# Performance work log

Hardware: AMD Instinct MI355X
Metric: run time of the kernel (lower is better)

The kernel has to match this reference:

```python
import jax, jax.numpy as jnp
import numpy as np

N, IN_F, OUT_F, H = 8192, 256, 64, 4
NEG_SLOPE = 0.2


def setup_inputs() -> dict:
    key = jax.random.key(0)
    ks = jax.random.split(key, 8)
    inputs = jax.random.normal(ks[0], (N, IN_F), dtype=jnp.float32)
    # sparse-ish binary adjacency with self loops (sparse.softmax only sees nonzeros)
    adj = (jax.random.uniform(ks[1], (N, N)) < 0.05).astype(jnp.float32)
    idx = jnp.arange(N)
    adj = adj.at[idx, idx].set(1.0)
    stdv = 1.0 / np.sqrt(H * OUT_F)
    weight = jax.random.uniform(ks[2], (IN_F, H * OUT_F), minval=-stdv, maxval=stdv, dtype=jnp.float32)
    bias = jax.random.uniform(ks[3], (1, H * OUT_F), minval=-stdv, maxval=stdv, dtype=jnp.float32)
    # weight_u/v: stdv = 1/sqrt(size(-1)=1) = 1
    weight_u = jax.random.uniform(ks[4], (H, OUT_F, 1), minval=-1.0, maxval=1.0, dtype=jnp.float32)
    weight_v = jax.random.uniform(ks[5], (H, OUT_F, 1), minval=-1.0, maxval=1.0, dtype=jnp.float32)
    stdp = 1.0 / np.sqrt(IN_F)
    proj_w = jax.random.uniform(ks[6], (H * OUT_F, IN_F), minval=-stdp, maxval=stdp, dtype=jnp.float32)
    proj_b = jax.random.uniform(ks[7], (H * OUT_F,), minval=-stdp, maxval=stdp, dtype=jnp.float32)
    return {"inputs": inputs, "adj_mat": adj, "weight": weight, "weight_u": weight_u,
            "weight_v": weight_v, "bias": bias, "proj_w": proj_w, "proj_b": proj_b}


def reference(inputs, adj_mat, weight, weight_u, weight_v, bias, proj_w, proj_b):
    n = inputs.shape[0]
    support = (inputs @ weight).reshape(n, H, OUT_F).transpose(1, 0, 2)  # [H,N,O]
    f1 = jnp.einsum('hno,ho->hn', support, weight_u[..., 0])  # [H,N]
    f2 = jnp.einsum('hno,ho->hn', support, weight_v[..., 0])  # [H,N]
    logits = f1[:, None, :] + f2[:, :, None]                  # [H,N,N]
    w = jax.nn.leaky_relu(logits, NEG_SLOPE)
    masked = w * adj_mat                                      # adj broadcast over heads
    mask = adj_mat != 0.0
    # sparse.softmax over dim 2: softmax restricted to nonzero (edge) positions
    neg = jnp.where(mask, masked, -jnp.inf)
    m = jnp.max(neg, axis=2, keepdims=True)
    m = jnp.where(jnp.isfinite(m), m, 0.0)
    e = jnp.where(mask, jnp.exp(neg - m), 0.0)
    denom = jnp.sum(e, axis=2, keepdims=True)
    attn = e / jnp.where(denom > 0, denom, 1.0)               # [H,N,N]
    out = jnp.einsum('hnm,hmo->hno', attn, support)           # [H,N,O]
    out = out.transpose(1, 0, 2).reshape(n, H * OUT_F)
    out = out + bias
    out = out + inputs @ proj_w.T + proj_b
    return out
```

## Files before the change

### kernel.cpp

```cpp
#include <hip/hip_runtime.h>
#include <hip/hip_bf16.h>

#define N_NODES 8192
#define IN_FEAT 256
#define OUT_F   64
#define NHEAD   4
#define HF      256
#define NEG     0.2f

typedef unsigned short u16;
typedef unsigned char  u8;
typedef unsigned long long u64;
typedef _Float16 h2    __attribute__((ext_vector_type(2)));
typedef _Float16 half8 __attribute__((ext_vector_type(8)));
typedef __attribute__((ext_vector_type(4))) float f32x4;

__global__ __launch_bounds__(256) void k_tr(const float* __restrict__ PW,
                                            float* __restrict__ PWT) {
    __shared__ float t[64][65];
    const int bx = (blockIdx.x & 3) * 64;
    const int by = (blockIdx.x >> 2) * 64;
    const int tx = threadIdx.x & 63;
    const int ty = threadIdx.x >> 6;
    #pragma unroll
    for (int r = ty; r < 64; r += 4)
        t[r][tx] = PW[(size_t)(by + r) * IN_FEAT + bx + tx];
    __syncthreads();
    #pragma unroll
    for (int r = ty; r < 64; r += 4)
        PWT[(size_t)(bx + r) * HF + by + tx] = t[tx][r];
}

#define RPB 4
__global__ __launch_bounds__(256, 8) void k_gemm(
    const float* __restrict__ inp,
    const float* __restrict__ W,
    const float* __restrict__ U,
    const float* __restrict__ V,
    const float* __restrict__ Bias,
    const float* __restrict__ PWT,
    const float* __restrict__ PB,
    const float* __restrict__ adj,
    _Float16* __restrict__ suppB,
    float* __restrict__ f1,
    float* __restrict__ f2,
    float* __restrict__ outp,
    unsigned* __restrict__ gb32,
    float* __restrict__ anum,
    float* __restrict__ aden)
{
    __shared__ __align__(16) float in_lds[RPB][IN_FEAT];
    const int c  = threadIdx.x;
    const int n0 = blockIdx.x * RPB;

    #pragma unroll
    for (int r = 0; r < RPB; ++r)
        in_lds[r][c] = inp[(size_t)(n0 + r) * IN_FEAT + c];
    __syncthreads();

    float accs[RPB], accp[RPB];
    #pragma unroll
    for (int r = 0; r < RPB; ++r) { accs[r] = 0.f; accp[r] = 0.f; }

    const float* wc = W   + c;
    const float* pc = PWT + c;
    float w0 = wc[0 * HF], w1 = wc[1 * HF], w2 = wc[2 * HF], w3 = wc[3 * HF];
    float p0 = pc[0 * HF], p1 = pc[1 * HF], p2 = pc[2 * HF], p3 = pc[3 * HF];

    #pragma unroll 1
    for (int k = 0; k < IN_FEAT; k += 4) {
        const int kn = (k + 4) & 255;
        const float nw0 = wc[(kn + 0) * HF];
        const float nw1 = wc[(kn + 1) * HF];
        const float nw2 = wc[(kn + 2) * HF];
        const float nw3 = wc[(kn + 3) * HF];
        const float np0 = pc[(kn + 0) * HF];
        const float np1 = pc[(kn + 1) * HF];
        const float np2 = pc[(kn + 2) * HF];
        const float np3 = pc[(kn + 3) * HF];
        #pragma unroll
        for (int r = 0; r < RPB; ++r) {
            const float4 xv = *(const float4*)&in_lds[r][k];
            accs[r] = fmaf(xv.x, w0, accs[r]);
            accs[r] = fmaf(xv.y, w1, accs[r]);
            accs[r] = fmaf(xv.z, w2, accs[r]);
            accs[r] = fmaf(xv.w, w3, accs[r]);
            accp[r] = fmaf(xv.x, p0, accp[r]);
            accp[r] = fmaf(xv.y, p1, accp[r]);
            accp[r] = fmaf(xv.z, p2, accp[r]);
            accp[r] = fmaf(xv.w, p3, accp[r]);
        }
        w0 = nw0; w1 = nw1; w2 = nw2; w3 = nw3;
        p0 = np0; p1 = np1; p2 = np2; p3 = np3;
    }

    const int h = c >> 6, lane = c & 63;
    const float uv = U[c], vv = V[c];
    const float bb = Bias[c] + PB[c];

    {
        const int o   = c & 63;
        const int t   = o >> 4;
        const int cc  = o & 15;
        const int jbg = n0 >> 5;
        const int q   = (n0 & 31) >> 3;
        const int el  = n0 & 7;
        union { _Float16 hh[4]; u64 q8; } sv;
        #pragma unroll
        for (int r = 0; r < RPB; ++r) sv.hh[r] = (_Float16)accs[r];
        const size_t word = ((size_t)(h * 256 + jbg) * 4 + t) * 64 + (q << 4) + cc;
        *(u64*)(suppB + word * 8 + el) = sv.q8;
    }

    #pragma unroll
    for (int r = 0; r < RPB; ++r) {
        float s1 = accs[r] * uv, s2 = accs[r] * vv;
        #pragma unroll
        for (int mm = 32; mm > 0; mm >>= 1) {
            s1 += __shfl_xor(s1, mm);
            s2 += __shfl_xor(s2, mm);
        }
        if (lane == 0) {
            f1[h * N_NODES + n0 + r] = s1;
            f2[h * N_NODES + n0 + r] = s2;
        }
        outp[(size_t)(n0 + r) * HF + c] = accp[r] + bb;
    }

    #pragma unroll
    for (int r = 0; r < RPB; ++r)
        anum[(size_t)(n0 + r) * HF + c] = 0.f;
    if (c < 16)
        aden[(size_t)(c >> 2) * N_NODES + n0 + (c & 3)] = 0.f;

    #pragma unroll
    for (int r = 0; r < RPB; ++r) {
        const float* ar = adj + (size_t)(n0 + r) * N_NODES;
        unsigned wrd = 0;
        #pragma unroll
        for (int p = 0; p < 4; ++p) {
            const int j = c * 32 + p * 8;
            const float4 a0 = *(const float4*)(ar + j);
            const float4 a1 = *(const float4*)(ar + j + 4);
            const unsigned b =
                (unsigned)(a0.x != 0.f)        | ((unsigned)(a0.y != 0.f) << 1) |
                ((unsigned)(a0.z != 0.f) << 2) | ((unsigned)(a0.w != 0.f) << 3) |
                ((unsigned)(a1.x != 0.f) << 4) | ((unsigned)(a1.y != 0.f) << 5) |
                ((unsigned)(a1.z != 0.f) << 6) | ((unsigned)(a1.w != 0.f) << 7);
            wrd |= b << (8 * p);
        }
        gb32[(size_t)(n0 + r) * 256 + c] = wrd;
    }
}

__global__ __launch_bounds__(256) void k_prep(const float* __restrict__ f1,
                                              float* __restrict__ f1max,
                                              _Float16* __restrict__ EA16,
                                              _Float16* __restrict__ EB16) {
    __shared__ float red[256];
    const int h = blockIdx.x;
    float m = -1e30f;
    for (int j = threadIdx.x; j < N_NODES; j += 256)
        m = fmaxf(m, f1[h * N_NODES + j]);
    red[threadIdx.x] = m;
    __syncthreads();
    for (int s = 128; s > 0; s >>= 1) {
        if (threadIdx.x < s) red[threadIdx.x] = fmaxf(red[threadIdx.x], red[threadIdx.x + s]);
        __syncthreads();
    }
    const float fm = red[0];
    if (threadIdx.x == 0) f1max[h] = fm;
    for (int j = threadIdx.x; j < N_NODES; j += 256) {
        const float d = f1[h * N_NODES + j] - fm;
        EA16[(size_t)h * N_NODES + j] = (_Float16)__expf(d);
        EB16[(size_t)h * N_NODES + j] = (_Float16)__expf(NEG * d);
    }
}

#define TI 64
#define NSUB 4
#define JSPLIT_G 4
#define JW (N_NODES / JSPLIT_G)

__global__ __launch_bounds__(256, 3) void k_attn_mfma(
    const unsigned* __restrict__ gb32,
    const _Float16* __restrict__ suppB,
    const _Float16* __restrict__ EA16,
    const _Float16* __restrict__ EB16,
    const float* __restrict__ f2,
    const float* __restrict__ f1max,
    float* __restrict__ anum,
    float* __restrict__ aden)
{
    __shared__ __align__(16) _Float16 ea_lds[NHEAD][JW];
    __shared__ __align__(16) _Float16 eb_lds[NHEAD][JW];
    __shared__ __align__(4)  u8 abyte[TI][260];

    const int itile = blockIdx.x >> 2;
    const int jwin  = blockIdx.x & 3;
    const int i0    = itile * TI;
    const int J0    = jwin * JW;
    const int wv    = threadIdx.x >> 6;
    const int lane  = threadIdx.x & 63;
    const int col   = lane & 15;
    const int quad  = lane >> 4;

    {
        const _Float16* gea = EA16 + (size_t)wv * N_NODES + J0;
        const _Float16* geb = EB16 + (size_t)wv * N_NODES + J0;
        #pragma unroll
        for (int it = 0; it < 4; ++it) {
            const int off = it * 512 + lane * 8;
            *(float4*)&ea_lds[wv][off] = *(const float4*)(gea + off);
            *(float4*)&eb_lds[wv][off] = *(const float4*)(geb + off);
        }
    }
    #pragma unroll
    for (int rr = 0; rr < 16; ++rr) {
        const int r = (wv << 4) + rr;
        *(unsigned*)&abyte[r][lane * 4] =
            gb32[(size_t)(i0 + r) * 256 + (J0 >> 5) + lane];
    }
    __syncthreads();

    const int h = wv;
    const float fm = f1max[h];
    h2 caH[NSUB], cbH[NSUB];
    float ls[NSUB];
    #pragma unroll
    for (int s = 0; s < NSUB; ++s) {
        const float f2i = f2[(size_t)h * N_NODES + i0 + s * 16 + col];
        const float g  = fm + f2i;
        const float mi = fmaxf(g, NEG * g);
        const _Float16 ca = (_Float16)__expf(g - mi);
        const _Float16 cb = (_Float16)__expf(NEG * g - mi);
        caH[s][0] = ca; caH[s][1] = ca;
        cbH[s][0] = cb; cbH[s][1] = cb;
        ls[s] = 0.f;
    }
    const h2 ones = {(_Float16)1.0f, (_Float16)1.0f};

    const _Float16* sb = suppB + (size_t)h * 524288
                       + (size_t)(J0 >> 5) * 2048 + lane * 8;

    f32x4 acc[NSUB][4];
    #pragma unroll
    for (int s = 0; s < NSUB; ++s)
        #pragma unroll
        for (int t = 0; t < 4; ++t)
            acc[s][t] = (f32x4){0.f, 0.f, 0.f, 0.f};

    const int qo = quad << 3;

    #pragma unroll 2
    for (int jb = 0; jb < JW; jb += 32) {
        const int jl = jb + qo;
        const _Float16* fp = sb + (size_t)(jb >> 5) * 2048;
        const half8 bv0 = *(const half8*)(fp);
        const half8 bv1 = *(const half8*)(fp + 512);
        const half8 bv2 = *(const half8*)(fp + 1024);
        const half8 bv3 = *(const half8*)(fp + 1536);

        union { half8 v; h2 pr[4]; } ea, eb;
        ea.v = *(const half8*)&ea_lds[h][jl];
        eb.v = *(const half8*)&eb_lds[h][jl];
        const int wo = (jb >> 3) + quad;

        #pragma unroll
        for (int s = 0; s < NSUB; ++s) {
            const unsigned gw = abyte[col + s * 16][wo];
            union { half8 v; unsigned w[4]; h2 pr[4]; } af;
            #pragma unroll
            for (int p = 0; p < 4; ++p) {
                const h2 pa = ea.pr[p] * caH[s];
                const h2 pb = eb.pr[p] * cbH[s];
                const h2 x  = __builtin_elementwise_max(pa, pb);
                const unsigned mlo = (unsigned)((int)(gw << (31 - 2 * p)) >> 31) & 0x0000FFFFu;
                const unsigned mhi = (unsigned)((int)(gw << (30 - 2 * p)) >> 31) & 0xFFFF0000u;
                union { h2 hh; unsigned u; } xu;
                xu.hh = x;
                xu.u &= (mlo | mhi);
                af.w[p] = xu.u;
                ls[s] = __builtin_amdgcn_fdot2(xu.hh, ones, ls[s], false);
            }
            acc[s][0] = __builtin_amdgcn_mfma_f32_16x16x32_f16(af.v, bv0, acc[s][0], 0, 0, 0);
            acc[s][1] = __builtin_amdgcn_mfma_f32_16x16x32_f16(af.v, bv1, acc[s][1], 0, 0, 0);
            acc[s][2] = __builtin_amdgcn_mfma_f32_16x16x32_f16(af.v, bv2, acc[s][2], 0, 0, 0);
            acc[s][3] = __builtin_amdgcn_mfma_f32_16x16x32_f16(af.v, bv3, acc[s][3], 0, 0, 0);
        }
    }

    #pragma unroll
    for (int s = 0; s < NSUB; ++s) {
        ls[s] += __shfl_xor(ls[s], 16);
        ls[s] += __shfl_xor(ls[s], 32);
    }
    if (quad == 0) {
        #pragma unroll
        for (int s = 0; s < NSUB; ++s)
            unsafeAtomicAdd(aden + (size_t)h * N_NODES + i0 + s * 16 + col, ls[s]);
    }

    #pragma unroll
    for (int s = 0; s < NSUB; ++s) {
        #pragma unroll
        for (int reg = 0; reg < 4; ++reg) {
            const int irow = (quad << 2) + reg;
            float* ap = anum + (size_t)(i0 + s * 16 + irow) * HF + (h << 6) + col;
            #pragma unroll
            for (int t = 0; t < 4; ++t)
                unsafeAtomicAdd(ap + (t << 4), acc[s][t][reg]);
        }
    }
}

__global__ __launch_bounds__(256) void k_fin(const float* __restrict__ anum,
                                             const float* __restrict__ aden,
                                             float* __restrict__ out) {
    const int c = threadIdx.x;
    const int h = c >> 6;
    #pragma unroll
    for (int rr = 0; rr < 4; ++rr) {
        const int n = blockIdx.x * 4 + rr;
        out[(size_t)n * HF + c] += anum[(size_t)n * HF + c]
                                 / aden[(size_t)h * N_NODES + n];
    }
}

extern "C" void kernel_launch(void* const* d_in, const int* in_sizes, int n_in,
                              void* d_out, int out_size, void* d_ws, size_t ws_size,
                              hipStream_t stream) {
    const float* inp  = (const float*)d_in[0];
    const float* adj  = (const float*)d_in[1];
    const float* W    = (const float*)d_in[2];
    const float* U    = (const float*)d_in[3];
    const float* V    = (const float*)d_in[4];
    const float* Bias = (const float*)d_in[5];
    const float* PW   = (const float*)d_in[6];
    const float* PB   = (const float*)d_in[7];
    float* out = (float*)d_out;

    char* ws = (char*)d_ws;
    _Float16* suppB = (_Float16*)(ws);
    float* f1    = (float*)(ws + (4u << 20));
    float* f2    = (float*)(ws + (4u << 20) + (128u << 10));
    float* f1mx  = (float*)(ws + (4u << 20) + (256u << 10));
    float* PWT   = (float*)(ws + (4u << 20) + (320u << 10));
    _Float16* EA16 = (_Float16*)(ws + (4u << 20) + (576u << 10));
    _Float16* EB16 = (_Float16*)(ws + (4u << 20) + (704u << 10));
    float* aden  = (float*)(ws + (4u << 20) + (832u << 10));
    unsigned* gb32 = (unsigned*)(ws + (8u << 20));
    float* anum  = (float*)(ws + (24u << 20));

    k_tr<<<16, 256, 0, stream>>>(PW, PWT);
    k_gemm<<<N_NODES / RPB, 256, 0, stream>>>(inp, W, U, V, Bias, PWT, PB, adj,
                                              suppB, f1, f2, out, gb32, anum, aden);
    k_prep<<<NHEAD, 256, 0, stream>>>(f1, f1mx, EA16, EB16);
    k_attn_mfma<<<(N_NODES / TI) * JSPLIT_G, 256, 0, stream>>>(
        gb32, suppB, EA16, EB16, f2, f1mx, anum, aden);
    k_fin<<<N_NODES / 4, 256, 0, stream>>>(anum, aden, out);
}
```

Baseline: 517.3 us.

## Move projection GEMMs to fp16 MFMA and split adjacency bitpacking into ballot kernel

Replaces the scalar fp32 FMA GEMM (support and projection) with fp16 MFMA 16x16x32, adding kernels that convert inputs to fp16 and pack W and proj_w into an MFMA-friendly layout. Adjacency bitmask construction moves into its own kernel using wavefront ballots, and zeroing of accumulators moves into the input conversion kernel. The aim is to cut the compute cost of the dense GEMM and to simplify the bitmask pass. In exchange it adds launches and lowers the GEMM to fp16 precision, including the residual projection path.

```diff
diff --git a/kernel.cpp b/kernel.cpp
--- a/kernel.cpp
+++ b/kernel.cpp
@@ -10,146 +10,174 @@
 
 typedef unsigned short u16;
 typedef unsigned char  u8;
+typedef unsigned int   u32;
 typedef unsigned long long u64;
 typedef _Float16 h2    __attribute__((ext_vector_type(2)));
 typedef _Float16 half8 __attribute__((ext_vector_type(8)));
 typedef __attribute__((ext_vector_type(4))) float f32x4;
 
-__global__ __launch_bounds__(256) void k_tr(const float* __restrict__ PW,
-                                            float* __restrict__ PWT) {
-    __shared__ float t[64][65];
-    const int bx = (blockIdx.x & 3) * 64;
-    const int by = (blockIdx.x >> 2) * 64;
-    const int tx = threadIdx.x & 63;
-    const int ty = threadIdx.x >> 6;
-    #pragma unroll
-    for (int r = ty; r < 64; r += 4)
-        t[r][tx] = PW[(size_t)(by + r) * IN_FEAT + bx + tx];
-    __syncthreads();
-    #pragma unroll
-    for (int r = ty; r < 64; r += 4)
-        PWT[(size_t)(bx + r) * HF + by + tx] = t[tx][r];
-}
-
-#define RPB 4
-__global__ __launch_bounds__(256, 8) void k_gemm(
-    const float* __restrict__ inp,
-    const float* __restrict__ W,
+__global__ __launch_bounds__(256) void k_x16(const float* __restrict__ inp,
+                                             _Float16* __restrict__ X16,
+                                             float* __restrict__ anum,
+                                             float* __restrict__ aden) {
+    const int i = blockIdx.x * 256 + threadIdx.x;
+    const float4 v = ((const float4*)inp)[i];
+    union { _Float16 hh[4]; u64 q; } cv;
+    cv.hh[0] = (_Float16)v.x; cv.hh[1] = (_Float16)v.y;
+    cv.hh[2] = (_Float16)v.z; cv.hh[3] = (_Float16)v.w;
+    ((u64*)X16)[i] = cv.q;
+    ((float4*)anum)[i] = (float4){0.f, 0.f, 0.f, 0.f};
+    if (i < 8192) ((float4*)aden)[i] = (float4){0.f, 0.f, 0.f, 0.f};
+}
+
+__global__ __launch_bounds__(256) void k_wpack(const float* __restrict__ W,
+                                               const float* __restrict__ PW,
+                                               _Float16* __restrict__ W16B) {
+    const int w = blockIdx.x * 256 + threadIdx.x;
+    const int ks = w >> 11;
+    const int T  = (w >> 6) & 31;
+    const int lane = w & 63;
+    const int q  = lane >> 4, cc = lane & 15;
+    const int n  = T * 16 + cc;
+    const int k0 = ks * 32 + q * 8;
+    union { _Float16 hh[8]; half8 v; } o;
+    #pragma unroll
+    for (int e = 0; e < 8; ++e) {
+        const int k = k0 + e;
+        const float s = (n < 256) ? W[k * 256 + n] : PW[(size_t)(n - 256) * 256 + k];
+        o.hh[e] = (_Float16)s;
+    }
+    *(half8*)(W16B + (size_t)w * 8) = o.v;
+}
+
+__global__ __launch_bounds__(256) void k_bits(const float* __restrict__ adj,
+                                              u64* __restrict__ gb64) {
+    const int row  = blockIdx.x * 4 + (threadIdx.x >> 6);
+    const int lane = threadIdx.x & 63;
+    const float* ar = adj + (size_t)row * N_NODES;
+    u64* gr = gb64 + (size_t)row * 128;
+    #pragma unroll 1
+    for (int it = 0; it < 32; ++it) {
+        const int jb = it * 256;
+        const float a0 = ar[jb + lane];
+        const float a1 = ar[jb + 64 + lane];
+        const float a2 = ar[jb + 128 + lane];
+        const float a3 = ar[jb + 192 + lane];
+        const u64 b0 = __ballot(a0 != 0.f);
+        const u64 b1 = __ballot(a1 != 0.f);
+        const u64 b2 = __ballot(a2 != 0.f);
+        const u64 b3 = __ballot(a3 != 0.f);
+        if (lane == 0) {
+            gr[it * 4 + 0] = b0; gr[it * 4 + 1] = b1;
+            gr[it * 4 + 2] = b2; gr[it * 4 + 3] = b3;
+        }
+    }
+}
+
+#define GROWS 16
+__global__ __launch_bounds__(256) void k_gemm(
+    const _Float16* __restrict__ X16,
+    const _Float16* __restrict__ W16B,
     const float* __restrict__ U,
     const float* __restrict__ V,
     const float* __restrict__ Bias,
-    const float* __restrict__ PWT,
     const float* __restrict__ PB,
-    const float* __restrict__ adj,
     _Float16* __restrict__ suppB,
     float* __restrict__ f1,
     float* __restrict__ f2,
-    float* __restrict__ outp,
-    unsigned* __restrict__ gb32,
-    float* __restrict__ anum,
-    float* __restrict__ aden)
+    float* __restrict__ outp)
 {
-    __shared__ __align__(16) float in_lds[RPB][IN_FEAT];
-    const int c  = threadIdx.x;
-    const int n0 = blockIdx.x * RPB;
-
-    #pragma unroll
-    for (int r = 0; r < RPB; ++r)
-        in_lds[r][c] = inp[(size_t)(n0 + r) * IN_FEAT + c];
+    __shared__ __align__(16) _Float16 xl[GROWS][264];
+    const int n0  = blockIdx.x * GROWS;
+    const int tid = threadIdx.x;
+    const int wv  = tid >> 6, lane = tid & 63;
+    const int col = lane & 15, quad = lane >> 4;
+
+    {
+        const int r = tid >> 4, seg = tid & 15;
+        const half8* src = (const half8*)(X16 + (size_t)(n0 + r) * 256 + seg * 16);
+        *(half8*)&xl[r][seg * 16]     = src[0];
+        *(half8*)&xl[r][seg * 16 + 8] = src[1];
+    }
     __syncthreads();
 
-    float accs[RPB], accp[RPB];
-    #pragma unroll
-    for (int r = 0; r < RPB; ++r) { accs[r] = 0.f; accp[r] = 0.f; }
-
-    const float* wc = W   + c;
-    const float* pc = PWT + c;
-    float w0 = wc[0 * HF], w1 = wc[1 * HF], w2 = wc[2 * HF], w3 = wc[3 * HF];
-    float p0 = pc[0 * HF], p1 = pc[1 * HF], p2 = pc[2 * HF], p3 = pc[3 * HF];
-
-    #pragma unroll 1
-    for (int k = 0; k < IN_FEAT; k += 4) {
-        const int kn = (k + 4) & 255;
-        const float nw0 = wc[(kn + 0) * HF];
-        const float nw1 = wc[(kn + 1) * HF];
-        const float nw2 = wc[(kn + 2) * HF];
-        const float nw3 = wc[(kn + 3) * HF];
-        const float np0 = pc[(kn + 0) * HF];
-        const float np1 = pc[(kn + 1) * HF];
-        const float np2 = pc[(kn + 2) * HF];
-        const float np3 = pc[(kn + 3) * HF];
-        #pragma unroll
-        for (int r = 0; r < RPB; ++r) {
-            const float4 xv = *(const float4*)&in_lds[r][k];
-            accs[r] = fmaf(xv.x, w0, accs[r]);
-            accs[r] = fmaf(xv.y, w1, accs[r]);
-            accs[r] = fmaf(xv.z, w2, accs[r]);
-            accs[r] = fmaf(xv.w, w3, accs[r]);
-            accp[r] = fmaf(xv.x, p0, accp[r]);
-            accp[r] = fmaf(xv.y, p1, accp[r]);
-            accp[r] = fmaf(xv.z, p2, accp[r]);
-            accp[r] = fmaf(xv.w, p3, accp[r]);
-        }
-        w0 = nw0; w1 = nw1; w2 = nw2; w3 = nw3;
-        p0 = np0; p1 = np1; p2 = np2; p3 = np3;
-    }
-
-    const int h = c >> 6, lane = c & 63;
-    const float uv = U[c], vv = V[c];
-    const float bb = Bias[c] + PB[c];
-
-    {
-        const int o   = c & 63;
-        const int t   = o >> 4;
-        const int cc  = o & 15;
+    f32x4 acc[8];
+    #pragma unroll
+    for (int t = 0; t < 8; ++t) acc[t] = (f32x4){0.f, 0.f, 0.f, 0.f};
+
+    const int qo = quad * 8;
+    #pragma unroll
+    for (int ks = 0; ks < 8; ++ks) {
+        const half8 af = *(const half8*)&xl[col][ks * 32 + qo];
+        const _Float16* bb = W16B + ((size_t)(ks * 32 + wv * 8) * 64 + lane) * 8;
+        #pragma unroll
+        for (int t = 0; t < 8; ++t) {
+            const half8 bw = *(const half8*)(bb + (size_t)t * 512);
+            acc[t] = __builtin_amdgcn_mfma_f32_16x16x32_f16(af, bw, acc[t], 0, 0, 0);
+        }
+    }
+
+    if (wv < 2) {
         const int jbg = n0 >> 5;
-        const int q   = (n0 & 31) >> 3;
-        const int el  = n0 & 7;
-        union { _Float16 hh[4]; u64 q8; } sv;
-        #pragma unroll
-        for (int r = 0; r < RPB; ++r) sv.hh[r] = (_Float16)accs[r];
-        const size_t word = ((size_t)(h * 256 + jbg) * 4 + t) * 64 + (q << 4) + cc;
-        *(u64*)(suppB + word * 8 + el) = sv.q8;
-    }
-
-    #pragma unroll
-    for (int r = 0; r < RPB; ++r) {
-        float s1 = accs[r] * uv, s2 = accs[r] * vv;
-        #pragma unroll
-        for (int mm = 32; mm > 0; mm >>= 1) {
-            s1 += __shfl_xor(s1, mm);
-            s2 += __shfl_xor(s2, mm);
-        }
-        if (lane == 0) {
-            f1[h * N_NODES + n0 + r] = s1;
-            f2[h * N_NODES + n0 + r] = s2;
-        }
-        outp[(size_t)(n0 + r) * HF + c] = accp[r] + bb;
-    }
-
-    #pragma unroll
-    for (int r = 0; r < RPB; ++r)
-        anum[(size_t)(n0 + r) * HF + c] = 0.f;
-    if (c < 16)
-        aden[(size_t)(c >> 2) * N_NODES + n0 + (c & 3)] = 0.f;
-
-    #pragma unroll
-    for (int r = 0; r < RPB; ++r) {
-        const float* ar = adj + (size_t)(n0 + r) * N_NODES;
-        unsigned wrd = 0;
-        #pragma unroll
-        for (int p = 0; p < 4; ++p) {
-            const int j = c * 32 + p * 8;
-            const float4 a0 = *(const float4*)(ar + j);
-            const float4 a1 = *(const float4*)(ar + j + 4);
-            const unsigned b =
-                (unsigned)(a0.x != 0.f)        | ((unsigned)(a0.y != 0.f) << 1) |
-                ((unsigned)(a0.z != 0.f) << 2) | ((unsigned)(a0.w != 0.f) << 3) |
-                ((unsigned)(a1.x != 0.f) << 4) | ((unsigned)(a1.y != 0.f) << 5) |
-                ((unsigned)(a1.z != 0.f) << 6) | ((unsigned)(a1.w != 0.f) << 7);
-            wrd |= b << (8 * p);
-        }
-        gb32[(size_t)(n0 + r) * 256 + c] = wrd;
+        const int nlo = n0 & 31;
+        #pragma unroll
+        for (int t = 0; t < 8; ++t) {
+            const int cg = wv * 128 + t * 16 + col;
+            const int h  = cg >> 6;
+            const int tp = (cg >> 4) & 3;
+            #pragma unroll
+            for (int reg = 0; reg < 4; ++reg) {
+                const int irow = quad * 4 + reg;
+                const int j31  = nlo + irow;
+                const size_t word = ((size_t)(h * 256 + jbg) * 4 + tp) * 64
+                                  + ((j31 >> 3) << 4) + col;
+                suppB[word * 8 + (j31 & 7)] = (_Float16)acc[t][reg];
+            }
+        }
+        float s1a[4] = {0,0,0,0}, s2a[4] = {0,0,0,0};
+        float s1b[4] = {0,0,0,0}, s2b[4] = {0,0,0,0};
+        #pragma unroll
+        for (int t = 0; t < 8; ++t) {
+            const int cg = wv * 128 + t * 16 + col;
+            const float uu = U[cg], vv = V[cg];
+            #pragma unroll
+            for (int reg = 0; reg < 4; ++reg) {
+                if (t < 4) { s1a[reg] += acc[t][reg] * uu; s2a[reg] += acc[t][reg] * vv; }
+                else       { s1b[reg] += acc[t][reg] * uu; s2b[reg] += acc[t][reg] * vv; }
+            }
+        }
+        #pragma unroll
+        for (int m = 1; m < 16; m <<= 1) {
+            #pragma unroll
+            for (int reg = 0; reg < 4; ++reg) {
+                s1a[reg] += __shfl_xor(s1a[reg], m);
+                s2a[reg] += __shfl_xor(s2a[reg], m);
+                s1b[reg] += __shfl_xor(s1b[reg], m);
+                s2b[reg] += __shfl_xor(s2b[reg], m);
+            }
+        }
+        if (col == 0) {
+            const int hA = wv * 2, hB = wv * 2 + 1;
+            #pragma unroll
+            for (int reg = 0; reg < 4; ++reg) {
+                const int n = n0 + quad * 4 + reg;
+                f1[hA * N_NODES + n] = s1a[reg];
+                f2[hA * N_NODES + n] = s2a[reg];
+                f1[hB * N_NODES + n] = s1b[reg];
+                f2[hB * N_NODES + n] = s2b[reg];
+            }
+        }
+    } else {
+        #pragma unroll
+        for (int t = 0; t < 8; ++t) {
+            const int cg = (wv - 2) * 128 + t * 16 + col;
+            const float bb2 = Bias[cg] + PB[cg];
+            #pragma unroll
+            for (int reg = 0; reg < 4; ++reg) {
+                const int irow = quad * 4 + reg;
+                outp[(size_t)(n0 + irow) * HF + cg] = acc[t][reg] + bb2;
+            }
+        }
     }
 }
 
@@ -345,18 +373,21 @@
     float* f1    = (float*)(ws + (4u << 20));
     float* f2    = (float*)(ws + (4u << 20) + (128u << 10));
     float* f1mx  = (float*)(ws + (4u << 20) + (256u << 10));
-    float* PWT   = (float*)(ws + (4u << 20) + (320u << 10));
     _Float16* EA16 = (_Float16*)(ws + (4u << 20) + (576u << 10));
     _Float16* EB16 = (_Float16*)(ws + (4u << 20) + (704u << 10));
     float* aden  = (float*)(ws + (4u << 20) + (832u << 10));
-    unsigned* gb32 = (unsigned*)(ws + (8u << 20));
+    u64*   gb64  = (u64*)(ws + (8u << 20));
+    _Float16* X16  = (_Float16*)(ws + (16u << 20));
+    _Float16* W16B = (_Float16*)(ws + (20u << 20));
     float* anum  = (float*)(ws + (24u << 20));
 
-    k_tr<<<16, 256, 0, stream>>>(PW, PWT);
-    k_gemm<<<N_NODES / RPB, 256, 0, stream>>>(inp, W, U, V, Bias, PWT, PB, adj,
-                                              suppB, f1, f2, out, gb32, anum, aden);
-    k_prep<<<NHEAD, 256, 0, stream>>>(f1, f1mx, EA16, EB16);
+    k_x16  <<<2048, 256, 0, stream>>>(inp, X16, anum, aden);
+    k_wpack<<<  64, 256, 0, stream>>>(W, PW, W16B);
+    k_bits <<<2048, 256, 0, stream>>>(adj, gb64);
+    k_gemm <<< 512, 256, 0, stream>>>(X16, W16B, U, V, Bias, PB,
+                                      suppB, f1, f2, out);
+    k_prep <<<NHEAD, 256, 0, stream>>>(f1, f1mx, EA16, EB16);
     k_attn_mfma<<<(N_NODES / TI) * JSPLIT_G, 256, 0, stream>>>(
-        gb32, suppB, EA16, EB16, f2, f1mx, anum, aden);
-    k_fin<<<N_NODES / 4, 256, 0, stream>>>(anum, aden, out);
-}
+        (const unsigned*)gb64, suppB, EA16, EB16, f2, f1mx, anum, aden);
+    k_fin  <<<N_NODES / 4, 256, 0, stream>>>(anum, aden, out);
+}
```

Measured after the change: 487.8 us. -5.7%, faster.
